# Performance work log

Hardware: AMD Instinct MI355X
Metric: run time of the kernel (lower is better)

The kernel has to match this reference:

```python
import jax, jax.numpy as jnp
import numpy as np

EPS = 1e-8  # torch.cosine_similarity default eps


def setup_inputs() -> dict:
    key = jax.random.key(0)
    k1, k2, k3 = jax.random.split(key, 3)
    B, N, M, C = 8, 2048, 2048, 128
    z = jax.random.randint(k1, (B, N, M), 0, 3, dtype=jnp.int32) - 1  # values in {-1,0,1}
    x1 = jax.random.normal(k2, (B, N, C), dtype=jnp.float32)
    x2 = jax.random.normal(k3, (B, M, C), dtype=jnp.float32)
    s = 10.0
    t = jnp.asarray(s, dtype=jnp.float32)   # nn.Parameter(s)
    b = jnp.asarray(-s, dtype=jnp.float32)  # nn.Parameter(-s)
    return {"z": z, "x1": x1, "x2": x2, "t": t, "b": b}


def reference(z, x1, x2, t, b):
    # cosine similarity as a GEMM instead of broadcast O(B*N*M*C) product:
    # cos = (x1 . x2) / max(||x1|| * ||x2||, eps)  (matches torch.cosine_similarity)
    dots = jnp.einsum('bnc,bmc->bnm', x1, x2)            # [B,N,M]
    n1 = jnp.sqrt(jnp.sum(x1 * x1, axis=-1))             # [B,N]
    n2 = jnp.sqrt(jnp.sum(x2 * x2, axis=-1))             # [B,M]
    denom = jnp.maximum(n1[:, :, None] * n2[:, None, :], EPS)
    cos_sim = dots / denom                               # [B,N,M]

    y = z.astype(jnp.float32) * (t * cos_sim - b)
    mask = z != 0
    nll = -jax.nn.log_sigmoid(y)
    loss = jnp.sum(jnp.where(mask, nll, 0.0)) / jnp.sum(mask).astype(jnp.float32)
    return loss, cos_sim, mask
```

## Files before the change

### kernel.cpp

```cpp
#include <hip/hip_runtime.h>
#include <hip/hip_bf16.h>

#define BATCH 8
#define NDIM  2048
#define MDIM  2048
#define CDIM  128

typedef __attribute__((ext_vector_type(8))) short bf16x8;
typedef __attribute__((ext_vector_type(4))) float f32x4;
typedef __attribute__((ext_vector_type(4), aligned(4))) float f32x4u;

__device__ __forceinline__ float bf2f(unsigned int u16){
    union { unsigned int u; float f; } v; v.u = u16 << 16; return v.f;
}
__device__ __forceinline__ unsigned int f2bf(float f){
    union { float f; unsigned int u; } v; v.f = f;
    unsigned int u = v.u;
    u += 0x7FFFu + ((u >> 16) & 1u);
    return u >> 16;
}

__global__ void ws_init_kernel(unsigned int* wsu){
    wsu[threadIdx.x] = 0u;
}

__global__ void finalize_kernel(const float* wsf, float* out){
    float s = 0.f;
    int   c = 0;
    #pragma unroll
    for (int i = 0; i < 32; ++i){
        s += wsf[i];
        c += ((const int*)wsf)[32 + i];
    }
    out[0] = s / (float)c;
}

__global__ __launch_bounds__(256, 5) void cossim_bce_main(
    const int*  __restrict__ zp,
    const float* __restrict__ x1,
    const float* __restrict__ x2,
    const float* __restrict__ tparm,
    const float* __restrict__ bparm,
    float* __restrict__ out,
    float* __restrict__ wsf)
{
    __shared__ __align__(16) unsigned short lds[(64 + 128) * 64];
    __shared__ float nsh[192];
    unsigned short* lA = lds;
    unsigned short* lB = lds + 64*64;

    const int t  = threadIdx.x;
    const int bx = blockIdx.x;
    const int by = blockIdx.y;
    const int bz = blockIdx.z;

    const float tv = *tparm;
    const float bv = *bparm;

    const float* x1base = x1 + ((size_t)(bz*NDIM) + by*64 ) * CDIM;
    const float* x2base = x2 + ((size_t)(bz*MDIM) + bx*128) * CDIM;

    const int lane = t & 63;
    const int w    = t >> 6;
    const int quad = lane >> 4;
    const int l16  = lane & 15;
    const int hi   = lane >> 5;
    const int c4   = lane & 31;

    f32x4 acc[8];
    #pragma unroll
    for (int n = 0; n < 8; ++n)
        acc[n] = (f32x4){0.f, 0.f, 0.f, 0.f};

    float nsum = 0.f;

    #pragma unroll
    for (int ph = 0; ph < 2; ++ph){
        #pragma unroll
        for (int i = 0; i < 6; ++i){
            int chunk = i*256 + t;
            const float* srcb;
            uint4* dst;
            int row, pos;
            if (i < 2){
                row = chunk >> 3; pos = chunk & 7;
                srcb = x1base; dst = (uint4*)lA;
            } else {
                int c2 = chunk - 512;
                row = c2 >> 3; pos = c2 & 7;
                srcb = x2base; dst = (uint4*)lB;
            }
            const float* p = srcb + row*CDIM + ph*64 + pos*8;
            float4 a = *(const float4*)p;
            float4 b = *(const float4*)(p + 4);
            uint4 pk;
            pk.x = f2bf(a.x) | (f2bf(a.y) << 16);
            pk.y = f2bf(a.z) | (f2bf(a.w) << 16);
            pk.z = f2bf(b.x) | (f2bf(b.y) << 16);
            pk.w = f2bf(b.z) | (f2bf(b.w) << 16);
            dst[row*8 + (pos ^ (row & 7))] = pk;
        }
        __syncthreads();

        #pragma unroll
        for (int kk = 0; kk < 2; ++kk){
            const int kc = kk*4 + quad;
            const int arow = w*16 + l16;
            bf16x8 afr = ((const bf16x8*)lA)[arow*8 + (kc ^ (arow & 7))];
            #pragma unroll
            for (int g = 0; g < 2; ++g){
                bf16x8 bfr[4];
                #pragma unroll
                for (int nn = 0; nn < 4; ++nn){
                    int brow = (g*4 + nn)*16 + l16;
                    bfr[nn] = ((const bf16x8*)lB)[brow*8 + (kc ^ (brow & 7))];
                }
                #pragma unroll
                for (int nn = 0; nn < 4; ++nn)
                    acc[g*4+nn] = __builtin_amdgcn_mfma_f32_16x16x32_bf16(
                                    afr, bfr[nn], acc[g*4+nn], 0, 0, 0);
            }
        }

        if (t < 192){
            const uint4* base; int row;
            if (t < 64){ base = (const uint4*)lA; row = t; }
            else       { base = (const uint4*)lB; row = t - 64; }
            #pragma unroll
            for (int c = 0; c < 8; ++c){
                uint4 v = base[row*8 + (c ^ (row & 7))];
                float f0 = bf2f(v.x & 0xffffu), f1 = bf2f(v.x >> 16);
                float f2 = bf2f(v.y & 0xffffu), f3 = bf2f(v.y >> 16);
                float f4 = bf2f(v.z & 0xffffu), f5 = bf2f(v.z >> 16);
                float f6 = bf2f(v.w & 0xffffu), f7 = bf2f(v.w >> 16);
                nsum += f0*f0 + f1*f1 + f2*f2 + f3*f3 + f4*f4 + f5*f5 + f6*f6 + f7*f7;
            }
        }
        __syncthreads();
    }

    if (t < 192) nsh[t] = 1.0f / sqrtf(fmaxf(nsum, 1e-16f));
    __syncthreads();

    float in1[4], in2[8];
    #pragma unroll
    for (int r = 0; r < 4; ++r) in1[r] = nsh[w*16 + quad*4 + r];
    #pragma unroll
    for (int n = 0; n < 8; ++n) in2[n] = nsh[64 + n*16 + l16];

    float* scr = (float*)lds + w*1024;
    float* cosOut  = out + 1;
    float* maskOut = out + 1 + (size_t)BATCH*NDIM*MDIM;
    const size_t rowBase = (size_t)bz*NDIM*MDIM + (size_t)(by*64 + w*16)*MDIM + (size_t)(bx*128);

    float lnum = 0.f;
    int   lcnt = 0;

    int4 zpre[4];
    #pragma unroll
    for (int i = 0; i < 4; ++i)
        zpre[i] = *(const int4*)(zp + rowBase + (size_t)(i*4 + hi)*MDIM + c4*4);

    #pragma unroll
    for (int rr = 0; rr < 2; ++rr){
        #pragma unroll
        for (int n = 0; n < 8; ++n){
            #pragma unroll
            for (int j = 0; j < 2; ++j){
                int r  = rr*2 + j;
                int sr = quad*2 + j;
                scr[sr*128 + ((n*16 + l16 + sr*4) & 127)] = acc[n][r] * in1[r] * in2[n];
            }
        }
        #pragma unroll
        for (int i = 0; i < 4; ++i){
            int sr  = i*2 + hi;
            int col = (c4*4 + sr*4) & 127;
            f32x4 cs4 = *(const f32x4*)(scr + sr*128 + col);
            int rowRel = i*4 + rr*2 + hi;
            size_t idx = rowBase + (size_t)rowRel*MDIM + c4*4;

            int4 z4 = zpre[i];
            if (rr == 0)
                zpre[i] = *(const int4*)(zp + idx + (size_t)2*MDIM);

            f32x4 mk;
            float nl = 0.f;
            int   nc = 0;
            #pragma unroll
            for (int j = 0; j < 4; ++j){
                int zv = (&z4.x)[j];
                float cs = cs4[j];
                mk[j] = zv ? 1.0f : 0.0f;
                float y  = (float)zv * (tv*cs - bv);
                float nll = fmaxf(-y, 0.f) + __logf(1.0f + __expf(-fabsf(y)));
                nl += zv ? nll : 0.f;
                nc += zv ? 1 : 0;
            }
            lnum += nl;
            lcnt += nc;
            *(f32x4u*)(cosOut  + idx) = cs4;
            *(f32x4u*)(maskOut + idx) = mk;
        }
    }

    #pragma unroll
    for (int off = 32; off > 0; off >>= 1){
        lnum += __shfl_down(lnum, off);
        lcnt += __shfl_down(lcnt, off);
    }
    __syncthreads();
    if (lane == 0){ nsh[w] = lnum; ((int*)nsh)[4 + w] = lcnt; }
    __syncthreads();
    if (t == 0){
        float s = nsh[0] + nsh[1] + nsh[2] + nsh[3];
        int   c = ((int*)nsh)[4] + ((int*)nsh)[5] + ((int*)nsh)[6] + ((int*)nsh)[7];
        int cell = (bx + by*16 + bz*512) & 31;
        atomicAdd(wsf + cell, s);
        atomicAdd((int*)wsf + 32 + cell, c);
    }
}

extern "C" void kernel_launch(void* const* d_in, const int* in_sizes, int n_in,
                              void* d_out, int out_size, void* d_ws, size_t ws_size,
                              hipStream_t stream) {
    const int*   zp = (const int*)  d_in[0];
    const float* x1 = (const float*)d_in[1];
    const float* x2 = (const float*)d_in[2];
    const float* tp = (const float*)d_in[3];
    const float* bp = (const float*)d_in[4];
    float* out = (float*)d_out;
    float* wsf = (float*)d_ws;

    ws_init_kernel<<<1, 64, 0, stream>>>((unsigned int*)d_ws);
    dim3 grid(MDIM/128, NDIM/64, BATCH);
    cossim_bce_main<<<grid, 256, 0, stream>>>(zp, x1, x2, tp, bp, out, wsf);
    finalize_kernel<<<1, 1, 0, stream>>>(wsf, out);
}
```

Measured before the change: 131.5 us.

## Precompute bf16 operands and inverse norms in a prep kernel, load via LDS DMA

Adds a prep kernel that converts x1/x2 to bf16 once and computes per-row inverse norms into workspace. The main kernel then streams bf16 tiles directly into LDS with global_load_lds, reads A fragments from global memory, and drops the per-block conversion and norm work. This removes redundant fp32 loads and conversion across blocks and shrinks LDS use, at the cost of an extra launch and an 8MB workspace round trip. It falls back to the old path if the workspace is too small.

```diff
diff --git a/kernel.cpp b/kernel.cpp
--- a/kernel.cpp
+++ b/kernel.cpp
@@ -20,19 +20,234 @@
     return u >> 16;
 }
 
-__global__ void ws_init_kernel(unsigned int* wsu){
-    wsu[threadIdx.x] = 0u;
-}
-
-__global__ void finalize_kernel(const float* wsf, float* out){
+__device__ __forceinline__ void gload_lds16(const void* g, void* l){
+    __builtin_amdgcn_global_load_lds(
+        (const __attribute__((address_space(1))) void*)g,
+        (__attribute__((address_space(3))) void*)l, 16, 0, 0);
+}
+
+__global__ void ws_init_kernel(unsigned int* cells){
+    cells[threadIdx.x] = 0u;
+}
+
+__global__ void finalize_kernel(const float* cells, float* out){
     float s = 0.f;
     int   c = 0;
     #pragma unroll
     for (int i = 0; i < 32; ++i){
-        s += wsf[i];
-        c += ((const int*)wsf)[32 + i];
+        s += cells[i];
+        c += ((const int*)cells)[32 + i];
     }
     out[0] = s / (float)c;
+}
+
+__global__ __launch_bounds__(256) void prep_kernel(
+    const float* __restrict__ x1, const float* __restrict__ x2,
+    unsigned short* __restrict__ xb, float* __restrict__ inv)
+{
+    int gt  = blockIdx.x*256 + threadIdx.x;
+    int row = gt >> 4;
+    int seg = gt & 15;
+    const float* src = (row < 16384) ? (x1 + (size_t)row*128)
+                                     : (x2 + (size_t)(row - 16384)*128);
+    float4 a = *(const float4*)(src + seg*8);
+    float4 b = *(const float4*)(src + seg*8 + 4);
+    uint4 pk;
+    pk.x = f2bf(a.x) | (f2bf(a.y) << 16);
+    pk.y = f2bf(a.z) | (f2bf(a.w) << 16);
+    pk.z = f2bf(b.x) | (f2bf(b.y) << 16);
+    pk.w = f2bf(b.z) | (f2bf(b.w) << 16);
+    ((uint4*)xb)[(size_t)row*16 + seg] = pk;
+
+    float f0 = bf2f(pk.x & 0xffffu), f1 = bf2f(pk.x >> 16);
+    float f2 = bf2f(pk.y & 0xffffu), f3 = bf2f(pk.y >> 16);
+    float f4 = bf2f(pk.z & 0xffffu), f5 = bf2f(pk.z >> 16);
+    float f6 = bf2f(pk.w & 0xffffu), f7 = bf2f(pk.w >> 16);
+    float s = f0*f0 + f1*f1 + f2*f2 + f3*f3 + f4*f4 + f5*f5 + f6*f6 + f7*f7;
+    s += __shfl_xor(s, 1);
+    s += __shfl_xor(s, 2);
+    s += __shfl_xor(s, 4);
+    s += __shfl_xor(s, 8);
+    if (seg == 0) inv[row] = 1.0f / sqrtf(fmaxf(s, 1e-16f));
+}
+
+__global__ __launch_bounds__(256, 5) void cossim_bce_fast(
+    const int*  __restrict__ zp,
+    const unsigned short* __restrict__ xb,
+    const float* __restrict__ inv,
+    const float* __restrict__ tparm,
+    const float* __restrict__ bparm,
+    float* __restrict__ out,
+    float* __restrict__ cells)
+{
+    __shared__ __align__(16) unsigned short lB[128*64];
+
+    const int t  = threadIdx.x;
+    const int bx = blockIdx.x;
+    const int by = blockIdx.y;
+    const int bz = blockIdx.z;
+
+    const float tv = *tparm;
+    const float bv = *bparm;
+
+    const unsigned short* x1b = xb;
+    const unsigned short* x2b = xb + (size_t)16384*128;
+    const int x1r0 = bz*NDIM + by*64;
+    const int x2r0 = bz*MDIM + bx*128;
+
+    const int lane = t & 63;
+    const int w    = t >> 6;
+    const int quad = lane >> 4;
+    const int l16  = lane & 15;
+    const int hi   = lane >> 5;
+    const int c4   = lane & 31;
+
+    f32x4 acc[8];
+    #pragma unroll
+    for (int n = 0; n < 8; ++n)
+        acc[n] = (f32x4){0.f, 0.f, 0.f, 0.f};
+
+    const size_t rowBase = (size_t)bz*NDIM*MDIM + (size_t)(by*64 + w*16)*MDIM + (size_t)(bx*128);
+
+    #pragma unroll
+    for (int i = 0; i < 4; ++i){
+        int chunk = i*256 + t;
+        int row = chunk >> 3, pp = chunk & 7;
+        int srcpos = pp ^ (row & 7);
+        gload_lds16(x2b + ((size_t)(x2r0 + row))*128 + 0*64 + srcpos*8,
+                    lB + (size_t)(i*256 + w*64)*8);
+    }
+    __syncthreads();
+
+    float in1[4], in2[8];
+    #pragma unroll
+    for (int r = 0; r < 4; ++r) in1[r] = inv[x1r0 + w*16 + quad*4 + r];
+    #pragma unroll
+    for (int n = 0; n < 8; ++n) in2[n] = inv[16384 + x2r0 + n*16 + l16];
+
+    const unsigned short* aRow = x1b + ((size_t)(x1r0 + w*16 + l16))*128 + quad*8;
+
+    #pragma unroll
+    for (int kk = 0; kk < 2; ++kk){
+        bf16x8 afr = *(const bf16x8*)(aRow + kk*32);
+        const int kc = kk*4 + quad;
+        #pragma unroll
+        for (int g = 0; g < 2; ++g){
+            bf16x8 bfr[4];
+            #pragma unroll
+            for (int nn = 0; nn < 4; ++nn){
+                int brow = (g*4 + nn)*16 + l16;
+                bfr[nn] = ((const bf16x8*)lB)[brow*8 + (kc ^ (brow & 7))];
+            }
+            #pragma unroll
+            for (int nn = 0; nn < 4; ++nn)
+                acc[g*4+nn] = __builtin_amdgcn_mfma_f32_16x16x32_bf16(
+                                afr, bfr[nn], acc[g*4+nn], 0, 0, 0);
+        }
+    }
+    __syncthreads();
+
+    #pragma unroll
+    for (int i = 0; i < 4; ++i){
+        int chunk = i*256 + t;
+        int row = chunk >> 3, pp = chunk & 7;
+        int srcpos = pp ^ (row & 7);
+        gload_lds16(x2b + ((size_t)(x2r0 + row))*128 + 1*64 + srcpos*8,
+                    lB + (size_t)(i*256 + w*64)*8);
+    }
+    int4 zpre[4];
+    #pragma unroll
+    for (int i = 0; i < 4; ++i)
+        zpre[i] = *(const int4*)(zp + rowBase + (size_t)(i*4 + hi)*MDIM + c4*4);
+    __syncthreads();
+
+    #pragma unroll
+    for (int kk = 0; kk < 2; ++kk){
+        bf16x8 afr = *(const bf16x8*)(aRow + 64 + kk*32);
+        const int kc = kk*4 + quad;
+        #pragma unroll
+        for (int g = 0; g < 2; ++g){
+            bf16x8 bfr[4];
+            #pragma unroll
+            for (int nn = 0; nn < 4; ++nn){
+                int brow = (g*4 + nn)*16 + l16;
+                bfr[nn] = ((const bf16x8*)lB)[brow*8 + (kc ^ (brow & 7))];
+            }
+            #pragma unroll
+            for (int nn = 0; nn < 4; ++nn)
+                acc[g*4+nn] = __builtin_amdgcn_mfma_f32_16x16x32_bf16(
+                                afr, bfr[nn], acc[g*4+nn], 0, 0, 0);
+        }
+    }
+    __syncthreads();
+
+    float* scr = (float*)lB + w*1024;
+    float* cosOut  = out + 1;
+    float* maskOut = out + 1 + (size_t)BATCH*NDIM*MDIM;
+
+    float lnum = 0.f;
+    int   lcnt = 0;
+
+    #pragma unroll
+    for (int rr = 0; rr < 2; ++rr){
+        #pragma unroll
+        for (int n = 0; n < 8; ++n){
+            #pragma unroll
+            for (int j = 0; j < 2; ++j){
+                int r  = rr*2 + j;
+                int sr = quad*2 + j;
+                scr[sr*128 + ((n*16 + l16 + sr*4) & 127)] = acc[n][r] * in1[r] * in2[n];
+            }
+        }
+        #pragma unroll
+        for (int i = 0; i < 4; ++i){
+            int sr  = i*2 + hi;
+            int col = (c4*4 + sr*4) & 127;
+            f32x4 cs4 = *(const f32x4*)(scr + sr*128 + col);
+            int rowRel = i*4 + rr*2 + hi;
+            size_t idx = rowBase + (size_t)rowRel*MDIM + c4*4;
+
+            int4 z4 = zpre[i];
+            if (rr == 0)
+                zpre[i] = *(const int4*)(zp + idx + (size_t)2*MDIM);
+
+            f32x4 mk;
+            float nl = 0.f;
+            int   nc = 0;
+            #pragma unroll
+            for (int j = 0; j < 4; ++j){
+                int zv = (&z4.x)[j];
+                float cs = cs4[j];
+                mk[j] = zv ? 1.0f : 0.0f;
+                float y  = (float)zv * (tv*cs - bv);
+                float nll = fmaxf(-y, 0.f) + __logf(1.0f + __expf(-fabsf(y)));
+                nl += zv ? nll : 0.f;
+                nc += zv ? 1 : 0;
+            }
+            lnum += nl;
+            lcnt += nc;
+            *(f32x4u*)(cosOut  + idx) = cs4;
+            *(f32x4u*)(maskOut + idx) = mk;
+        }
+    }
+
+    #pragma unroll
+    for (int off = 32; off > 0; off >>= 1){
+        lnum += __shfl_down(lnum, off);
+        lcnt += __shfl_down(lcnt, off);
+    }
+    __syncthreads();
+    float* redf = (float*)lB;
+    int*   redi = (int*)lB + 8;
+    if (lane == 0){ redf[w] = lnum; redi[w] = lcnt; }
+    __syncthreads();
+    if (t == 0){
+        float s = redf[0] + redf[1] + redf[2] + redf[3];
+        int   c = redi[0] + redi[1] + redi[2] + redi[3];
+        int cell = (bx + by*16 + bz*512) & 31;
+        atomicAdd(cells + cell, s);
+        atomicAdd((int*)cells + 32 + cell, c);
+    }
 }
 
 __global__ __launch_bounds__(256, 5) void cossim_bce_main(
@@ -230,10 +445,22 @@
     const float* tp = (const float*)d_in[3];
     const float* bp = (const float*)d_in[4];
     float* out = (float*)d_out;
-    float* wsf = (float*)d_ws;
-
-    ws_init_kernel<<<1, 64, 0, stream>>>((unsigned int*)d_ws);
+
+    const size_t WS_NEEDED = (size_t)8*1024*1024 + 32768*4 + 256;
     dim3 grid(MDIM/128, NDIM/64, BATCH);
-    cossim_bce_main<<<grid, 256, 0, stream>>>(zp, x1, x2, tp, bp, out, wsf);
-    finalize_kernel<<<1, 1, 0, stream>>>(wsf, out);
-}
+
+    if (ws_size >= WS_NEEDED){
+        unsigned short* xb  = (unsigned short*)d_ws;
+        float* inv   = (float*)((char*)d_ws + (size_t)8*1024*1024);
+        float* cells = inv + 32768;
+        ws_init_kernel<<<1, 64, 0, stream>>>((unsigned int*)cells);
+        prep_kernel<<<2048, 256, 0, stream>>>(x1, x2, xb, inv);
+        cossim_bce_fast<<<grid, 256, 0, stream>>>(zp, xb, inv, tp, bp, out, cells);
+        finalize_kernel<<<1, 1, 0, stream>>>(cells, out);
+    } else {
+        float* wsf = (float*)d_ws;
+        ws_init_kernel<<<1, 64, 0, stream>>>((unsigned int*)d_ws);
+        cossim_bce_main<<<grid, 256, 0, stream>>>(zp, x1, x2, tp, bp, out, wsf);
+        finalize_kernel<<<1, 1, 0, stream>>>(wsf, out);
+    }
+}
```

After: 123.2 us. 1.07x faster.
